# Kernel optimization log

Hardware: AMD Instinct MI355X
Metric: run time of the kernel (lower is better)

The kernel has to match this reference:

```python
import jax, jax.numpy as jnp
import numpy as np

B, N, D = 8, 9856, 256
HEADS = 8
WH, WW = 7, 11
HID = 512  # int(D * 2.0)
EPS = 1e-5


def layernorm(x, g, b):
    mu = jnp.mean(x, axis=-1, keepdims=True)
    var = jnp.mean(jnp.square(x - mu), axis=-1, keepdims=True)
    return (x - mu) * jax.lax.rsqrt(var + EPS) * g + b


def setup_inputs() -> dict:
    key = jax.random.key(0)
    ks = jax.random.split(key, 6)
    s = lambda k, shape: (jax.random.normal(k, shape, jnp.float32) * 0.02)
    return {
        "x": jax.random.normal(ks[0], (B, N, D), jnp.float32),
        "norm1_g": jnp.ones((D,), jnp.float32),
        "norm1_b": jnp.zeros((D,), jnp.float32),
        "in_proj_w": s(ks[1], (3 * D, D)),
        "in_proj_b": jnp.zeros((3 * D,), jnp.float32),
        "out_w": s(ks[2], (D, D)),
        "out_b": jnp.zeros((D,), jnp.float32),
        "norm2_g": jnp.ones((D,), jnp.float32),
        "norm2_b": jnp.zeros((D,), jnp.float32),
        "fc1_w": s(ks[3], (HID, D)),
        "fc1_b": jnp.zeros((HID,), jnp.float32),
        "fc2_w": s(ks[4], (D, HID)),
        "fc2_b": jnp.zeros((D,), jnp.float32),
        "h": 56,
        "w": 176,
    }


def reference(x, norm1_g, norm1_b, in_proj_w, in_proj_b, out_w, out_b,
              norm2_g, norm2_b, fc1_w, fc1_b, fc2_w, fc2_b, h, w):
    Bx, Nx, Dx = x.shape
    n_h, n_w = h // WH, w // WW  # chosen dims divide evenly -> pad_h = pad_w = 0
    hd = Dx // HEADS
    L = WH * WW  # 77 tokens per window

    res = x
    xn = layernorm(x, norm1_g, norm1_b)

    # window partition: (B, h*w, D) -> (B*n_h*n_w, wh*ww, D)
    win = xn.reshape(Bx, n_h, WH, n_w, WW, Dx)
    win = win.transpose(0, 1, 3, 2, 4, 5).reshape(-1, L, Dx)

    # MultiheadAttention (batch_first) on each window independently
    qkv = win @ in_proj_w.T + in_proj_b          # (NW, L, 3D)
    q, k, v = jnp.split(qkv, 3, axis=-1)
    NW = win.shape[0]
    q = q.reshape(NW, L, HEADS, hd).transpose(0, 2, 1, 3)
    k = k.reshape(NW, L, HEADS, hd).transpose(0, 2, 1, 3)
    v = v.reshape(NW, L, HEADS, hd).transpose(0, 2, 1, 3)
    scores = jnp.einsum("nhld,nhmd->nhlm", q, k) / jnp.sqrt(jnp.float32(hd))
    attn = jax.nn.softmax(scores, axis=-1)
    o = jnp.einsum("nhlm,nhmd->nhld", attn, v)   # (NW, H, L, hd)
    o = o.transpose(0, 2, 1, 3).reshape(NW, L, Dx)
    o = o @ out_w.T + out_b

    # window reverse: (B*n_h*n_w, wh*ww, D) -> (B, h*w, D)
    o = o.reshape(Bx, n_h, n_w, WH, WW, Dx)
    o = o.transpose(0, 1, 3, 2, 4, 5).reshape(Bx, Nx, Dx)

    x = res + o
    res = x
    xn2 = layernorm(x, norm2_g, norm2_b)
    hmid = jax.nn.gelu(xn2 @ fc1_w.T + fc1_b, approximate=False)
    mlp = hmid @ fc2_w.T + fc2_b
    return res + mlp
```

## Files before the change

### kernel.cpp

```cpp
#include <hip/hip_runtime.h>
#include <hip/hip_bf16.h>

typedef unsigned short u16;
typedef unsigned int   u32;

typedef __bf16 bf16x8 __attribute__((ext_vector_type(8)));
typedef float  f32x4  __attribute__((ext_vector_type(4)));

__device__ __forceinline__ u16 f2bf(float f) {
  u32 u = __float_as_uint(f);
  u += 0x7fffu + ((u >> 16) & 1u);
  return (u16)(u >> 16);
}
__device__ __forceinline__ u32 pack2(float a, float b) {
  return (u32)f2bf(a) | ((u32)f2bf(b) << 16);
}
__device__ __forceinline__ void gld16(const void* g, void* l) {
  __builtin_amdgcn_global_load_lds(
      (const __attribute__((address_space(1))) unsigned int*)g,
      (__attribute__((address_space(3))) unsigned int*)l, 16, 0, 0);
}

#define TOK_M   78848
#define DIM     256
#define NWIN    1024
#define WINL    77

__global__ __launch_bounds__(256)
void cvt_w(const float* __restrict__ w0, const float* __restrict__ w1,
           const float* __restrict__ w2, const float* __restrict__ w3,
           u16* __restrict__ out)
{
  const int i = (blockIdx.x * 256 + threadIdx.x) * 4;
  const float* src; int off;
  if      (i < 196608) { src = w0; off = i; }
  else if (i < 262144) { src = w1; off = i - 196608; }
  else if (i < 393216) { src = w2; off = i - 262144; }
  else                 { src = w3; off = i - 393216; }
  float4 v = *(const float4*)(src + off);
  uint2 o; o.x = pack2(v.x, v.y); o.y = pack2(v.z, v.w);
  *(uint2*)(out + i) = o;
}

template<bool PERM>
__global__ __launch_bounds__(256)
void ln_k(const float* __restrict__ X, const float* __restrict__ g,
          const float* __restrict__ bta, u16* __restrict__ Y)
{
  const int tid  = threadIdx.x;
  const int tok  = blockIdx.x * 4 + (tid >> 6);
  const int lane = tid & 63;
  float4 v = *(const float4*)(X + (size_t)tok * DIM + lane * 4);
  float s = v.x + v.y + v.z + v.w;
#pragma unroll
  for (int off = 32; off; off >>= 1) s += __shfl_xor(s, off);
  const float mu = s * (1.f / 256.f);
  const float dx = v.x - mu, dy = v.y - mu, dz = v.z - mu, dw = v.w - mu;
  float q = dx * dx + dy * dy + dz * dz + dw * dw;
#pragma unroll
  for (int off = 32; off; off >>= 1) q += __shfl_xor(q, off);
  const float rstd = rsqrtf(q * (1.f / 256.f) + 1e-5f);
  float4 gg = *(const float4*)(g + lane * 4);
  float4 bb = *(const float4*)(bta + lane * 4);
  const float y0 = dx * rstd * gg.x + bb.x;
  const float y1 = dy * rstd * gg.y + bb.y;
  const float y2 = dz * rstd * gg.z + bb.z;
  const float y3 = dw * rstd * gg.w + bb.w;
  size_t dest = (size_t)tok;
  if (PERM) {
    const int b  = tok / 9856, n = tok - b * 9856;
    const int y  = n / 176,  xc = n - y * 176;
    const int ih = y / 7,    rr = y - ih * 7;
    const int iw = xc / 11,  cc = xc - iw * 11;
    dest = (size_t)(((b * 8 + ih) * 16 + iw)) * 77 + rr * 11 + cc;
  }
  uint2 o;
  o.x = pack2(y0, y1);
  o.y = pack2(y2, y3);
  *(uint2*)(Y + dest * DIM + lane * 4) = o;
}

template<int EPI, int OBF>
__global__ __launch_bounds__(256, 3)
void gemm_mfma(const u16* __restrict__ A, const u16* __restrict__ W,
               const float* __restrict__ bias, const float* res,
               void* Cout, int N, int K)
{
  __shared__ u16 As[2][4096];
  __shared__ u16 Bs[2][4096];

  const int tid  = threadIdx.x;
  const int wave = tid >> 6, lane = tid & 63;
  const int wy = wave >> 1, wx = wave & 1;
  const int quad = lane >> 4, l16 = lane & 15;
  const int m0 = blockIdx.y * 128;
  const int n0 = blockIdx.x * 128;

  const int s0 = tid, s1 = tid + 256;
  const int r0 = s0 >> 2, r1 = s1 >> 2;
  const int kb0 = (s0 & 3) ^ (r0 & 3);
  const int kb1 = (s1 & 3) ^ (r1 & 3);
  const u16* Ag0 = A + (size_t)(m0 + r0) * K + kb0 * 8;
  const u16* Ag1 = A + (size_t)(m0 + r1) * K + kb1 * 8;
  const u16* Bg0 = W + (size_t)(n0 + r0) * K + kb0 * 8;
  const u16* Bg1 = W + (size_t)(n0 + r1) * K + kb1 * 8;

  const int kbs = quad ^ (l16 & 3);
  const int aoff = (wy * 64 + l16) * 32 + kbs * 8;
  const int boff = (wx * 64 + l16) * 32 + kbs * 8;

  f32x4 acc[4][4];
#pragma unroll
  for (int i = 0; i < 4; ++i)
#pragma unroll
    for (int j = 0; j < 4; ++j) {
      f32x4 z = {0.f, 0.f, 0.f, 0.f};
      acc[i][j] = z;
    }

  gld16(Ag0, &As[0][s0 * 8]);
  gld16(Ag1, &As[0][s1 * 8]);
  gld16(Bg0, &Bs[0][s0 * 8]);
  gld16(Bg1, &Bs[0][s1 * 8]);
  __syncthreads();

  const int NT = K >> 5;
  for (int t = 0; t < NT; ++t) {
    const int cur = t & 1;
    if (t + 1 < NT) {
      const int kt = (t + 1) << 5;
      gld16(Ag0 + kt, &As[cur ^ 1][s0 * 8]);
      gld16(Ag1 + kt, &As[cur ^ 1][s1 * 8]);
      gld16(Bg0 + kt, &Bs[cur ^ 1][s0 * 8]);
      gld16(Bg1 + kt, &Bs[cur ^ 1][s1 * 8]);
    }
    const u16* Ar = &As[cur][aoff];
    const u16* Br = &Bs[cur][boff];
    bf16x8 af[4], bv[4];
#pragma unroll
    for (int i = 0; i < 4; ++i) {
      af[i] = *(const bf16x8*)(Ar + i * 16 * 32);
      bv[i] = *(const bf16x8*)(Br + i * 16 * 32);
    }
#pragma unroll
    for (int mi = 0; mi < 4; ++mi)
#pragma unroll
      for (int ni = 0; ni < 4; ++ni)
        acc[mi][ni] = __builtin_amdgcn_mfma_f32_16x16x32_bf16(
            af[mi], bv[ni], acc[mi][ni], 0, 0, 0);
    __syncthreads();
  }

  const int gr0 = m0 + wy * 64 + quad * 4;
  const int gc0 = n0 + wx * 64 + l16;
#pragma unroll
  for (int ni = 0; ni < 4; ++ni) {
    const int gc = gc0 + ni * 16;
    const float bvs = bias[gc];
#pragma unroll
    for (int mi = 0; mi < 4; ++mi) {
      const int gr = gr0 + mi * 16;
      f32x4 a = acc[mi][ni];
#pragma unroll
      for (int e = 0; e < 4; ++e) {
        float v = a[e] + bvs;
        const size_t idx = (size_t)(gr + e) * N + gc;
        if (EPI == 1) v += res[idx];
        else if (EPI == 2) v = 0.5f * v * (1.f + erff(v * 0.70710678118654752f));
        if (OBF) ((u16*)Cout)[idx] = f2bf(v);
        else     ((float*)Cout)[idx] = v;
      }
    }
  }
}

#define PSTR 104
__global__ __launch_bounds__(128)
void attn_mfma(const u16* __restrict__ qkv, u16* __restrict__ onat)
{
  __shared__ __bf16 Pb[2][80 * PSTR];

  const int tid  = threadIdx.x;
  const int wave = tid >> 6, lane = tid & 63;
  const int quad = lane >> 4, l16 = lane & 15;
  const int pair = blockIdx.x * 2 + wave;
  const int nw   = pair >> 3, head = pair & 7;
  const size_t base = (size_t)nw * 77 * 768;
  const int hoff = head * 32;
  __bf16* P = Pb[wave];

  {
    uint4 z = {0, 0, 0, 0};
    for (int r = lane; r < 80; r += 64) {
      *(uint4*)(P + r * PSTR + 80) = z;
      *(uint4*)(P + r * PSTR + 88) = z;
    }
  }

  bf16x8 qf[5], kf[5];
  const u16* qp = qkv + base + hoff + quad * 8;
#pragma unroll
  for (int mi = 0; mi < 5; ++mi) {
    const size_t row = (size_t)(l16 + 16 * mi) * 768;
    qf[mi] = *(const bf16x8*)(qp + row);
    kf[mi] = *(const bf16x8*)(qp + row + 256);
  }

  f32x4 s[5][5];
#pragma unroll
  for (int mi = 0; mi < 5; ++mi)
#pragma unroll
    for (int ni = 0; ni < 5; ++ni) {
      f32x4 z = {0.f, 0.f, 0.f, 0.f};
      s[mi][ni] = z;
    }
#pragma unroll
  for (int mi = 0; mi < 5; ++mi)
#pragma unroll
    for (int ni = 0; ni < 5; ++ni)
      s[mi][ni] = __builtin_amdgcn_mfma_f32_16x16x32_bf16(
          qf[mi], kf[ni], s[mi][ni], 0, 0, 0);

  bf16x8 vf[3][2];
  {
    const __bf16* vbb = (const __bf16*)(qkv + base + 512 + hoff + l16);
#pragma unroll
    for (int ks = 0; ks < 3; ++ks)
#pragma unroll
      for (int ni = 0; ni < 2; ++ni)
#pragma unroll
        for (int jj = 0; jj < 8; ++jj) {
          const int k = ks * 32 + quad * 8 + jj;
          vf[ks][ni][jj] = (k < 77) ? vbb[(size_t)k * 768 + 16 * ni] : (__bf16)0.f;
        }
  }

  if (l16 >= 13) {
#pragma unroll
    for (int mi = 0; mi < 5; ++mi)
#pragma unroll
      for (int e = 0; e < 4; ++e) s[mi][4][e] = -1e30f;
  }

  const float c = 0.17677669529663687f * 1.4426950408889634f;
  float inv[5][4];
#pragma unroll
  for (int mi = 0; mi < 5; ++mi)
#pragma unroll
    for (int e = 0; e < 4; ++e) {
      float mx = s[mi][0][e];
#pragma unroll
      for (int ni = 1; ni < 5; ++ni) mx = fmaxf(mx, s[mi][ni][e]);
#pragma unroll
      for (int off = 1; off < 16; off <<= 1) mx = fmaxf(mx, __shfl_xor(mx, off));
      float sum = 0.f;
#pragma unroll
      for (int ni = 0; ni < 5; ++ni) {
        const float ev = exp2f((s[mi][ni][e] - mx) * c);
        s[mi][ni][e] = ev;
        sum += ev;
      }
#pragma unroll
      for (int off = 1; off < 16; off <<= 1) sum += __shfl_xor(sum, off);
      inv[mi][e] = 1.f / sum;
    }

#pragma unroll
  for (int mi = 0; mi < 5; ++mi)
#pragma unroll
    for (int e = 0; e < 4; ++e) {
      const int m = quad * 4 + e + 16 * mi;
#pragma unroll
      for (int ni = 0; ni < 5; ++ni)
        P[m * PSTR + l16 + 16 * ni] = (__bf16)(s[mi][ni][e] * inv[mi][e]);
    }

  f32x4 o[5][2];
#pragma unroll
  for (int mi = 0; mi < 5; ++mi)
#pragma unroll
    for (int ni = 0; ni < 2; ++ni) {
      f32x4 z = {0.f, 0.f, 0.f, 0.f};
      o[mi][ni] = z;
    }
#pragma unroll
  for (int ks = 0; ks < 3; ++ks)
#pragma unroll
    for (int mi = 0; mi < 5; ++mi) {
      const bf16x8 af = *(const bf16x8*)(P + (l16 + 16 * mi) * PSTR + ks * 32 + quad * 8);
#pragma unroll
      for (int ni = 0; ni < 2; ++ni)
        o[mi][ni] = __builtin_amdgcn_mfma_f32_16x16x32_bf16(
            af, vf[ks][ni], o[mi][ni], 0, 0, 0);
    }

  const int b  = nw >> 7;
  const int ih = (nw >> 4) & 7;
  const int iw = nw & 15;
#pragma unroll
  for (int mi = 0; mi < 5; ++mi)
#pragma unroll
    for (int e = 0; e < 4; ++e) {
      const int t = quad * 4 + e + 16 * mi;
      if (t < 77) {
        const int rr = t / 11, cc = t - rr * 11;
        const int y = ih * 7 + rr, xc = iw * 11 + cc;
        const size_t nat = (size_t)b * 9856 + (size_t)y * 176 + xc;
        u16* dst = onat + nat * DIM + hoff + l16;
        dst[0]  = f2bf(o[mi][0][e]);
        dst[16] = f2bf(o[mi][1][e]);
      }
    }
}

extern "C" void kernel_launch(void* const* d_in, const int* in_sizes, int n_in,
                              void* d_out, int out_size, void* d_ws, size_t ws_size,
                              hipStream_t stream)
{
  (void)in_sizes; (void)n_in; (void)out_size; (void)ws_size;
  const float* x    = (const float*)d_in[0];
  const float* g1   = (const float*)d_in[1];
  const float* b1   = (const float*)d_in[2];
  const float* wqkv = (const float*)d_in[3];
  const float* bqkv = (const float*)d_in[4];
  const float* wout = (const float*)d_in[5];
  const float* bout = (const float*)d_in[6];
  const float* g2   = (const float*)d_in[7];
  const float* b2   = (const float*)d_in[8];
  const float* w1   = (const float*)d_in[9];
  const float* bf1  = (const float*)d_in[10];
  const float* w2   = (const float*)d_in[11];
  const float* bf2  = (const float*)d_in[12];

  char* ws = (char*)d_ws;
  u16*   qkv  = (u16*)(ws);
  u16*   xn   = (u16*)(ws + 121110528);
  u16*   onat = (u16*)(ws + 161480704);
  u16*   wb   = (u16*)(ws + 201850880);
  u16*   wqkv_b = wb;
  u16*   wout_b = wb + 196608;
  u16*   w1_b   = wb + 262144;
  u16*   w2_b   = wb + 393216;
  float* x2   = (float*)d_out;

  cvt_w<<<512, 256, 0, stream>>>(wqkv, wout, w1, w2, wb);
  ln_k<true><<<19712, 256, 0, stream>>>(x, g1, b1, xn);
  gemm_mfma<0, 1><<<dim3(6, 616), 256, 0, stream>>>(xn, wqkv_b, bqkv, nullptr, qkv, 768, 256);
  attn_mfma<<<4096, 128, 0, stream>>>(qkv, onat);
  gemm_mfma<1, 0><<<dim3(2, 616), 256, 0, stream>>>(onat, wout_b, bout, x, x2, 256, 256);
  ln_k<false><<<19712, 256, 0, stream>>>(x2, g2, b2, xn);
  gemm_mfma<2, 1><<<dim3(4, 616), 256, 0, stream>>>(xn, w1_b, bf1, nullptr, qkv, 512, 256);
  gemm_mfma<1, 0><<<dim3(2, 616), 256, 0, stream>>>(qkv, w2_b, bf2, x2, x2, 256, 512);
}
```

Baseline: 582.6 us.

## Fuse LayerNorm into QKV and FC1 GEMMs with pre-tiled bf16 weight images

Replaces the separate LayerNorm kernels and their bf16 intermediate buffer with a fused kernel. Each block normalizes 64 token rows straight into a swizzled LDS A-tile, then loops over all N panels while streaming weight tiles from a pre-tiled bf16 image that cvt_w now lays out in MFMA fragment order. The aim is to drop the write and re-read of the normalized activations and two kernel launches. In exchange the grid has fewer blocks with longer serial panel loops, uses a larger LDS footprint that may limit occupancy, and does less M-tile work per block (64 rows instead of 128).

```diff
diff --git a/kernel.cpp b/kernel.cpp
--- a/kernel.cpp
+++ b/kernel.cpp
@@ -26,58 +26,156 @@
 #define NWIN    1024
 #define WINL    77
 
+template<int K, int NF>
+__device__ __forceinline__ void cvt_chunk(const float* __restrict__ src,
+                                          u16* __restrict__ dst, int rel)
+{
+  constexpr int KT = K / 32;
+  constexpr int PN = NF * 16;
+  const int lane  = rel & 63;
+  const int g     = rel >> 6;
+  const int nf    = g % NF;
+  const int kt    = (g / NF) % KT;
+  const int panel = g / (NF * KT);
+  const int col   = panel * PN + nf * 16 + (lane & 15);
+  const int k0    = kt * 32 + (lane >> 4) * 8;
+  const float4 a = *(const float4*)(src + (size_t)col * K + k0);
+  const float4 b = *(const float4*)(src + (size_t)col * K + k0 + 4);
+  uint4 o;
+  o.x = pack2(a.x, a.y); o.y = pack2(a.z, a.w);
+  o.z = pack2(b.x, b.y); o.w = pack2(b.z, b.w);
+  *(uint4*)(dst + (size_t)rel * 8) = o;
+}
+__device__ __forceinline__ void cvt_plain(const float* __restrict__ src,
+                                          u16* __restrict__ dst, int rel)
+{
+  const int i = rel * 8;
+  const float4 a = *(const float4*)(src + i);
+  const float4 b = *(const float4*)(src + i + 4);
+  uint4 o;
+  o.x = pack2(a.x, a.y); o.y = pack2(a.z, a.w);
+  o.z = pack2(b.x, b.y); o.w = pack2(b.z, b.w);
+  *(uint4*)(dst + i) = o;
+}
+
 __global__ __launch_bounds__(256)
-void cvt_w(const float* __restrict__ w0, const float* __restrict__ w1,
-           const float* __restrict__ w2, const float* __restrict__ w3,
+void cvt_w(const float* __restrict__ wqkv, const float* __restrict__ wout,
+           const float* __restrict__ w1, const float* __restrict__ w2,
            u16* __restrict__ out)
 {
-  const int i = (blockIdx.x * 256 + threadIdx.x) * 4;
-  const float* src; int off;
-  if      (i < 196608) { src = w0; off = i; }
-  else if (i < 262144) { src = w1; off = i - 196608; }
-  else if (i < 393216) { src = w2; off = i - 262144; }
-  else                 { src = w3; off = i - 393216; }
-  float4 v = *(const float4*)(src + off);
-  uint2 o; o.x = pack2(v.x, v.y); o.y = pack2(v.z, v.w);
-  *(uint2*)(out + i) = o;
-}
-
-template<bool PERM>
-__global__ __launch_bounds__(256)
-void ln_k(const float* __restrict__ X, const float* __restrict__ g,
-          const float* __restrict__ bta, u16* __restrict__ Y)
-{
+  const int c = blockIdx.x * 256 + threadIdx.x;
+  if      (c < 24576) cvt_chunk<256, 8>(wqkv, out,          c);
+  else if (c < 32768) cvt_plain(wout, out + 196608, c - 24576);
+  else if (c < 49152) cvt_chunk<256, 8>(w1,   out + 262144, c - 32768);
+  else                cvt_plain(w2,   out + 393216, c - 49152);
+}
+
+template<int NPAN, int EPI, int OBF, int PERM>
+__global__ __launch_bounds__(256, 3)
+void lngemm(const float* __restrict__ X, const u16* __restrict__ Wimg,
+            const float* __restrict__ lg, const float* __restrict__ lb,
+            const float* __restrict__ bias, void* __restrict__ Cout)
+{
+  constexpr int K  = 256;
+  constexpr int KT = K / 32;
+  constexpr int N  = NPAN * 128;
+  __shared__ u16 At[64 * K];
+  __shared__ u16 Bs[2][4096];
+
   const int tid  = threadIdx.x;
-  const int tok  = blockIdx.x * 4 + (tid >> 6);
-  const int lane = tid & 63;
-  float4 v = *(const float4*)(X + (size_t)tok * DIM + lane * 4);
-  float s = v.x + v.y + v.z + v.w;
-#pragma unroll
-  for (int off = 32; off; off >>= 1) s += __shfl_xor(s, off);
-  const float mu = s * (1.f / 256.f);
-  const float dx = v.x - mu, dy = v.y - mu, dz = v.z - mu, dw = v.w - mu;
-  float q = dx * dx + dy * dy + dz * dz + dw * dw;
-#pragma unroll
-  for (int off = 32; off; off >>= 1) q += __shfl_xor(q, off);
-  const float rstd = rsqrtf(q * (1.f / 256.f) + 1e-5f);
-  float4 gg = *(const float4*)(g + lane * 4);
-  float4 bb = *(const float4*)(bta + lane * 4);
-  const float y0 = dx * rstd * gg.x + bb.x;
-  const float y1 = dy * rstd * gg.y + bb.y;
-  const float y2 = dz * rstd * gg.z + bb.z;
-  const float y3 = dw * rstd * gg.w + bb.w;
-  size_t dest = (size_t)tok;
-  if (PERM) {
-    const int b  = tok / 9856, n = tok - b * 9856;
-    const int y  = n / 176,  xc = n - y * 176;
-    const int ih = y / 7,    rr = y - ih * 7;
-    const int iw = xc / 11,  cc = xc - iw * 11;
-    dest = (size_t)(((b * 8 + ih) * 16 + iw)) * 77 + rr * 11 + cc;
-  }
-  uint2 o;
-  o.x = pack2(y0, y1);
-  o.y = pack2(y2, y3);
-  *(uint2*)(Y + dest * DIM + lane * 4) = o;
+  const int wave = tid >> 6, lane = tid & 63;
+  const int quad = lane >> 4, l16 = lane & 15;
+  const int wy = wave >> 1, wx = wave & 1;
+  const int rowbase = blockIdx.x * 64;
+
+  {
+    const float4 gg = *(const float4*)(lg + lane * 4);
+    const float4 bb = *(const float4*)(lb + lane * 4);
+    const int c  = lane * 4;
+    const int kt = c >> 5, kb = (c >> 3) & 3, ko = c & 7;
+    for (int r = 0; r < 16; ++r) {
+      const int row = wave * 16 + r;
+      const float4 v = *(const float4*)(X + (size_t)(rowbase + row) * 256 + c);
+      float s = v.x + v.y + v.z + v.w;
+#pragma unroll
+      for (int off = 32; off; off >>= 1) s += __shfl_xor(s, off);
+      const float mu = s * (1.f / 256.f);
+      const float dx = v.x - mu, dy = v.y - mu, dz = v.z - mu, dw = v.w - mu;
+      float q = dx * dx + dy * dy + dz * dz + dw * dw;
+#pragma unroll
+      for (int off = 32; off; off >>= 1) q += __shfl_xor(q, off);
+      const float rstd = rsqrtf(q * (1.f / 256.f) + 1e-5f);
+      uint2 o;
+      o.x = pack2(dx * rstd * gg.x + bb.x, dy * rstd * gg.y + bb.y);
+      o.y = pack2(dz * rstd * gg.z + bb.z, dw * rstd * gg.w + bb.w);
+      *(uint2*)(At + row * 256 + kt * 32 + ((kb ^ (row & 3)) * 8) + ko) = o;
+    }
+  }
+  gld16(Wimg + tid * 8,        Bs[0] + tid * 8);
+  gld16(Wimg + 2048 + tid * 8, Bs[0] + 2048 + tid * 8);
+  __syncthreads();
+
+  int step = 0;
+  for (int np = 0; np < NPAN; ++np) {
+    f32x4 acc[2][4];
+#pragma unroll
+    for (int mi = 0; mi < 2; ++mi)
+#pragma unroll
+      for (int ni = 0; ni < 4; ++ni) {
+        f32x4 z = {0.f, 0.f, 0.f, 0.f};
+        acc[mi][ni] = z;
+      }
+#pragma unroll
+    for (int kt = 0; kt < KT; ++kt, ++step) {
+      const int cur = step & 1;
+      if (step + 1 < NPAN * KT) {
+        const u16* src = Wimg + (size_t)(step + 1) * 4096;
+        gld16(src + tid * 8,        Bs[cur ^ 1] + tid * 8);
+        gld16(src + 2048 + tid * 8, Bs[cur ^ 1] + 2048 + tid * 8);
+      }
+      bf16x8 af[2], bv[4];
+#pragma unroll
+      for (int mi = 0; mi < 2; ++mi)
+        af[mi] = *(const bf16x8*)(At + (wy * 32 + mi * 16 + l16) * 256 +
+                                  kt * 32 + (quad ^ (l16 & 3)) * 8);
+#pragma unroll
+      for (int ni = 0; ni < 4; ++ni)
+        bv[ni] = *(const bf16x8*)(Bs[cur] + ((wx * 4 + ni) * 64 + lane) * 8);
+#pragma unroll
+      for (int mi = 0; mi < 2; ++mi)
+#pragma unroll
+        for (int ni = 0; ni < 4; ++ni)
+          acc[mi][ni] = __builtin_amdgcn_mfma_f32_16x16x32_bf16(
+              af[mi], bv[ni], acc[mi][ni], 0, 0, 0);
+      __syncthreads();
+    }
+    const int col0 = np * 128 + wx * 64 + l16;
+#pragma unroll
+    for (int mi = 0; mi < 2; ++mi) {
+      const int r = rowbase + wy * 32 + mi * 16 + quad * 4;
+#pragma unroll
+      for (int e = 0; e < 4; ++e) {
+        const int gr = r + e;
+        size_t orow = (size_t)gr;
+        if (PERM) {
+          const int b  = gr / 9856, n = gr - b * 9856;
+          const int y  = n / 176,  xc = n - y * 176;
+          const int ih = y / 7,    rr = y - ih * 7;
+          const int iw = xc / 11,  cc = xc - iw * 11;
+          orow = (size_t)(((b * 8 + ih) * 16 + iw)) * 77 + rr * 11 + cc;
+        }
+#pragma unroll
+        for (int ni = 0; ni < 4; ++ni) {
+          const int col = col0 + ni * 16;
+          float v = acc[mi][ni][e] + bias[col];
+          if (EPI == 2) v = 0.5f * v * (1.f + erff(v * 0.70710678118654752f));
+          const size_t idx = orow * N + col;
+          if (OBF) ((u16*)Cout)[idx] = f2bf(v);
+          else     ((float*)Cout)[idx] = v;
+        }
+      }
+    }
+  }
 }
 
 template<int EPI, int OBF>
@@ -334,7 +432,6 @@
 
   char* ws = (char*)d_ws;
   u16*   qkv  = (u16*)(ws);
-  u16*   xn   = (u16*)(ws + 121110528);
   u16*   onat = (u16*)(ws + 161480704);
   u16*   wb   = (u16*)(ws + 201850880);
   u16*   wqkv_b = wb;
@@ -343,12 +440,10 @@
   u16*   w2_b   = wb + 393216;
   float* x2   = (float*)d_out;
 
-  cvt_w<<<512, 256, 0, stream>>>(wqkv, wout, w1, w2, wb);
-  ln_k<true><<<19712, 256, 0, stream>>>(x, g1, b1, xn);
-  gemm_mfma<0, 1><<<dim3(6, 616), 256, 0, stream>>>(xn, wqkv_b, bqkv, nullptr, qkv, 768, 256);
+  cvt_w<<<256, 256, 0, stream>>>(wqkv, wout, w1, w2, wb);
+  lngemm<6, 0, 1, 1><<<1232, 256, 0, stream>>>(x, wqkv_b, g1, b1, bqkv, qkv);
   attn_mfma<<<4096, 128, 0, stream>>>(qkv, onat);
   gemm_mfma<1, 0><<<dim3(2, 616), 256, 0, stream>>>(onat, wout_b, bout, x, x2, 256, 256);
-  ln_k<false><<<19712, 256, 0, stream>>>(x2, g2, b2, xn);
-  gemm_mfma<2, 1><<<dim3(4, 616), 256, 0, stream>>>(xn, w1_b, bf1, nullptr, qkv, 512, 256);
+  lngemm<4, 2, 1, 0><<<1232, 256, 0, stream>>>(x2, w1_b, g2, b2, bf1, qkv);
   gemm_mfma<1, 0><<<dim3(2, 616), 256, 0, stream>>>(qkv, w2_b, bf2, x2, x2, 256, 512);
 }
```

Result: no change. 575.0 us (-1.3%).
